# Optimization experiments

Hardware: AMD Instinct MI355X
Metric: run time of the kernel (lower is better)

The kernel has to match this reference:

```python
import jax, jax.numpy as jnp
import numpy as np

LN_EPS = 1e-5
BN_EPS = 1e-5
ALPHA = 0.1

def _layer_norm(x):
    # F.layer_norm over last dim, no affine
    mu = jnp.mean(x, axis=-1, keepdims=True)
    var = jnp.var(x, axis=-1, keepdims=True)
    return (x - mu) * jax.lax.rsqrt(var + LN_EPS)

def setup_inputs() -> dict:
    key = jax.random.key(0)
    ks = jax.random.split(key, 12)
    N, Nh, D, Dq = 8192, 8192, 64, 64
    s = 1.0 / np.sqrt(D)
    inp = {
        "X": jax.random.normal(ks[0], (N, D), jnp.float32),
        "H": jax.random.normal(ks[1], (Nh, D), jnp.float32),
        "M": jax.random.uniform(ks[2], (N, Nh), jnp.float32),
        # Linear params (torch nn.Linear: y = x @ W.T + b), uniform init scale
        "Qw": jax.random.uniform(ks[3], (Dq, D), jnp.float32, -s, s),
        "Qb": jax.random.uniform(ks[4], (Dq,), jnp.float32, -s, s),
        "Kw": jax.random.uniform(ks[5], (Dq, D), jnp.float32, -s, s),
        "Kb": jax.random.uniform(ks[6], (Dq,), jnp.float32, -s, s),
        "Vw": jax.random.uniform(ks[7], (64, D), jnp.float32, -s, s),
        "Vb": jax.random.uniform(ks[8], (64,), jnp.float32, -s, s),
        # BatchNorm1d(64) eval-mode params
        "bn_gamma": jnp.ones((64,), jnp.float32),
        "bn_beta": jnp.zeros((64,), jnp.float32),
        "bn_mean": 0.1 * jax.random.normal(ks[9], (64,), jnp.float32),
        "bn_var": jax.random.uniform(ks[10], (64,), jnp.float32, 0.5, 1.5),
    }
    return inp

def reference(X, H, M, Qw, Qb, Kw, Kb, Vw, Vb, bn_gamma, bn_beta, bn_mean, bn_var):
    # K/Q branches: Linear + LayerNorm
    K = _layer_norm(H @ Kw.T + Kb)            # [Nh, Dq]
    Q = _layer_norm(X @ Qw.T + Qb)            # [N, Dq]
    # V branch: Linear + BatchNorm1d (eval mode; dropout is identity in eval)
    V = (H @ Vw.T + Vb - bn_mean) * jax.lax.rsqrt(bn_var + BN_EPS) * bn_gamma + bn_beta  # [Nh, 64]
    # Masked attention, softmax over dim=0 (columns)
    A = (Q @ K.T) * 0.125                     # [N, Nh]
    A = jax.nn.softmax(M * A, axis=0)
    # globel=True branch
    return ALPHA * (A @ V) + M @ H            # [N, 64]
```

## Files before the change

kernel.cpp:

```cpp
#include <hip/hip_runtime.h>
#include <hip/hip_bf16.h>
#include <math.h>

#define NN 8192
#define QSCALE (0.125f * 1.44269504088896f)
#define OSZ (8192*64)
#define NSL 16

typedef __attribute__((ext_vector_type(8))) short short8;
typedef __attribute__((ext_vector_type(16))) float f32x16;
typedef __attribute__((ext_vector_type(4))) float f32x4;

union W4 { unsigned u[4]; short8 v; };

__device__ inline unsigned short f2bf(float x) {
  union { float f; unsigned u; } t; t.f = x;
  unsigned r = t.u + 0x7fffu + ((t.u >> 16) & 1u);
  return (unsigned short)(r >> 16);
}
__device__ inline unsigned cvtpk(float lo, float hi) {
  unsigned r;
  asm("v_cvt_pk_bf16_f32 %0, %1, %2" : "=v"(r) : "v"(lo), "v"(hi));
  return r;
}
__device__ inline float fexp2(float x) {
  float r;
  asm("v_exp_f32 %0, %1" : "=v"(r) : "v"(x));
  return r;
}
__device__ inline void gload16(const float* g, float* l) {
  __builtin_amdgcn_global_load_lds(
      (const __attribute__((address_space(1))) void*)g,
      (__attribute__((address_space(3))) void*)l, 16, 0, 0);
}

__global__ __launch_bounds__(256) void qkv_kernel(
    const float* __restrict__ X, const float* __restrict__ H,
    const float* __restrict__ Qw, const float* __restrict__ Qb,
    const float* __restrict__ Kw, const float* __restrict__ Kb,
    const float* __restrict__ Vw, const float* __restrict__ Vb,
    const float* __restrict__ bng, const float* __restrict__ bnb,
    const float* __restrict__ bnm, const float* __restrict__ bnv,
    unsigned short* __restrict__ QP, unsigned short* __restrict__ KP,
    unsigned short* __restrict__ VP, unsigned short* __restrict__ HP)
{
  int wid = (blockIdx.x * blockDim.x + threadIdx.x) >> 6;
  int d = threadIdx.x & 63;
  float4 w[16];

  for (int fq = 0; fq < 16; fq++) w[fq] = *(const float4*)(Qw + d*64 + fq*4);
  for (int rr = 0; rr < 4; rr++) {
    int r = wid*4 + rr;
    float a = Qb[d];
    for (int fq = 0; fq < 16; fq++) {
      float4 xv = *(const float4*)(X + r*64 + fq*4);
      a += w[fq].x*xv.x + w[fq].y*xv.y + w[fq].z*xv.z + w[fq].w*xv.w;
    }
    float s = a;
    for (int off = 32; off; off >>= 1) s += __shfl_xor(s, off);
    float mean = s * (1.f/64.f);
    float c = a - mean;
    float s2 = c*c;
    for (int off = 32; off; off >>= 1) s2 += __shfl_xor(s2, off);
    float q = c * rsqrtf(s2*(1.f/64.f) + 1e-5f);
    QP[(d>>3)*65536 + r*8 + (d&7)] = f2bf(q * QSCALE);
  }
  for (int fq = 0; fq < 16; fq++) w[fq] = *(const float4*)(Kw + d*64 + fq*4);
  for (int rr = 0; rr < 4; rr++) {
    int r = wid*4 + rr;
    float a = Kb[d];
    for (int fq = 0; fq < 16; fq++) {
      float4 hv = *(const float4*)(H + r*64 + fq*4);
      a += w[fq].x*hv.x + w[fq].y*hv.y + w[fq].z*hv.z + w[fq].w*hv.w;
    }
    float s = a;
    for (int off = 32; off; off >>= 1) s += __shfl_xor(s, off);
    float mean = s * (1.f/64.f);
    float c = a - mean;
    float s2 = c*c;
    for (int off = 32; off; off >>= 1) s2 += __shfl_xor(s2, off);
    float k = c * rsqrtf(s2*(1.f/64.f) + 1e-5f);
    KP[(d>>3)*65536 + r*8 + (d&7)] = f2bf(k);
  }
  for (int fq = 0; fq < 16; fq++) w[fq] = *(const float4*)(Vw + d*64 + fq*4);
  float bscale = rsqrtf(bnv[d] + 1e-5f) * bng[d];
  for (int rr = 0; rr < 4; rr++) {
    int r = wid*4 + rr;
    float a = Vb[d];
    for (int fq = 0; fq < 16; fq++) {
      float4 hv = *(const float4*)(H + r*64 + fq*4);
      a += w[fq].x*hv.x + w[fq].y*hv.y + w[fq].z*hv.z + w[fq].w*hv.w;
    }
    float v = (a - bnm[d]) * bscale + bnb[d];
    VP[(r>>3)*512 + d*8 + (r&7)] = f2bf(v);
    HP[(r>>3)*512 + d*8 + (r&7)] = f2bf(H[r*64 + d]);
  }
}

__global__ __launch_bounds__(256) void pass1_kernel(
    const float* __restrict__ M, const unsigned short* __restrict__ QP,
    const unsigned short* __restrict__ KP, float* __restrict__ pd)
{
  int tid = threadIdx.x;
  int wj = (blockIdx.x * blockDim.x + tid) >> 6;
  int lane = tid & 63;
  int l31 = lane & 31, h = lane >> 5;
  int jb = wj & 255, slice = wj >> 8;
  int j = jb*32 + l31;

  short8 kb[4];
  for (int m = 0; m < 4; m++)
    kb[m] = *(const short8*)(KP + (2*m + h)*65536 + j*8);

  float Mv[16];
  {
    int i0 = slice*8*32;
#pragma unroll
    for (int r = 0; r < 16; r++) {
      int ir = (r&3) + 8*(r>>2) + 4*h;
      Mv[r] = M[(size_t)(i0 + ir)*NN + j];
    }
  }

  float d0 = 0.f, d1 = 0.f, d2 = 0.f, d3 = 0.f;
  for (int t = 0; t < 8; t++) {
    int i0 = (slice*8 + t) * 32;
    float Mn[16];
    if (t < 7) {
      int i1 = i0 + 32;
#pragma unroll
      for (int r = 0; r < 16; r++) {
        int ir = (r&3) + 8*(r>>2) + 4*h;
        Mn[r] = M[(size_t)(i1 + ir)*NN + j];
      }
    }

    f32x16 acc;
    for (int r = 0; r < 16; r++) acc[r] = 0.f;
    __builtin_amdgcn_s_setprio(1);
    for (int m = 0; m < 4; m++) {
      short8 qa = *(const short8*)(QP + (2*m + h)*65536 + (size_t)(i0 + l31)*8);
      acc = __builtin_amdgcn_mfma_f32_32x32x16_bf16(qa, kb[m], acc, 0, 0, 0);
    }
    __builtin_amdgcn_s_setprio(0);

    d0 += fexp2(acc[0]*Mv[0]) + fexp2(acc[4]*Mv[4]) + fexp2(acc[8]*Mv[8])   + fexp2(acc[12]*Mv[12]);
    d1 += fexp2(acc[1]*Mv[1]) + fexp2(acc[5]*Mv[5]) + fexp2(acc[9]*Mv[9])   + fexp2(acc[13]*Mv[13]);
    d2 += fexp2(acc[2]*Mv[2]) + fexp2(acc[6]*Mv[6]) + fexp2(acc[10]*Mv[10]) + fexp2(acc[14]*Mv[14]);
    d3 += fexp2(acc[3]*Mv[3]) + fexp2(acc[7]*Mv[7]) + fexp2(acc[11]*Mv[11]) + fexp2(acc[15]*Mv[15]);

    if (t < 7) {
#pragma unroll
      for (int r = 0; r < 16; r++) Mv[r] = Mn[r];
    }
  }
  float drun = (d0 + d1) + (d2 + d3);
  drun += __shfl_xor(drun, 32);
  if (lane < 32) pd[(size_t)slice*NN + j] = drun;
}

__global__ __launch_bounds__(256) void cv_kernel(
    const float* __restrict__ pd, const unsigned short* __restrict__ VP,
    unsigned short* __restrict__ VP2)
{
  __shared__ float cls[256];
  int tid = threadIdx.x;
  int j = blockIdx.x * 256 + tid;
  float Dv = 0.f;
  for (int s = 0; s < 32; s++) Dv += pd[(size_t)s*NN + j];
  cls[tid] = 0.1f / Dv;
  __syncthreads();

  int base = blockIdx.x * 2048;
#pragma unroll
  for (int k = 0; k < 8; k++) {
    int idx = base + k*256 + tid;
    int lj8 = (k*256 + tid) >> 6;
    const unsigned short* src = VP + (size_t)idx*8;
    unsigned short sv[8];
    *(short8*)sv = *(const short8*)src;
    float f[8];
#pragma unroll
    for (int e = 0; e < 8; e++)
      f[e] = __uint_as_float(((unsigned)sv[e]) << 16) * cls[lj8*8 + e];
    W4 o;
    o.u[0] = cvtpk(f[0], f[1]); o.u[1] = cvtpk(f[2], f[3]);
    o.u[2] = cvtpk(f[4], f[5]); o.u[3] = cvtpk(f[6], f[7]);
    *(short8*)(VP2 + (size_t)idx*8) = o.v;
  }
}

__global__ __launch_bounds__(256) void pass2_kernel(
    const float* __restrict__ M, const unsigned short* __restrict__ QP,
    const unsigned short* __restrict__ KP, const unsigned short* __restrict__ VP2,
    const unsigned short* __restrict__ HP, float* __restrict__ opart)
{
  __shared__ __align__(16) float tile[2][128*32];

  int iblk = blockIdx.x >> 4, slice = blockIdx.x & 15;
  int i0 = iblk * 128;
  int tid = threadIdx.x;
  int lane = tid & 63, wv = tid >> 6;
  int l31 = lane & 31, h = lane >> 5;
  int irow = wv*32 + l31;
  int i_g = i0 + irow;
  int r7 = irow & 7;

  short8 qb[4];
#pragma unroll
  for (int m = 0; m < 4; m++)
    qb[m] = *(const short8*)(QP + (2*m + h)*65536 + (size_t)i_g*8);

  int rsub = lane >> 3;
  int gdst = lane & 7;
  int c0base = slice*512;

#pragma unroll
  for (int k = 0; k < 4; k++) {
    int rloc = wv*32 + k*8 + rsub;
    int gs = gdst ^ (rloc & 7);
    gload16(M + (size_t)(i0 + rloc)*NN + c0base + gs*4,
            &tile[0][(wv*32 + k*8)*32]);
  }

  f32x16 saccC;
  for (int r = 0; r < 16; r++) saccC[r] = 0.f;
  {
    short8 k0[4];
#pragma unroll
    for (int m = 0; m < 4; m++)
      k0[m] = *(const short8*)(KP + (2*m + h)*65536 + (size_t)(c0base + l31)*8);
    __builtin_amdgcn_s_setprio(1);
#pragma unroll
    for (int m = 0; m < 4; m++)
      saccC = __builtin_amdgcn_mfma_f32_32x32x16_bf16(k0[m], qb[m], saccC, 0, 0, 0);
    __builtin_amdgcn_s_setprio(0);
  }
  __syncthreads();

  f32x16 oaccA, oaccB;
  for (int r = 0; r < 16; r++) { oaccA[r] = 0.f; oaccB[r] = 0.f; }

  for (int tm = 0; tm < 16; tm++) {
    int jt = c0base + tm*32;

    if (tm < 15) {
      int c0 = c0base + (tm+1)*32;
      float* dst = tile[(tm+1) & 1];
#pragma unroll
      for (int k = 0; k < 4; k++) {
        int rloc = wv*32 + k*8 + rsub;
        int gs = gdst ^ (rloc & 7);
        gload16(M + (size_t)(i0 + rloc)*NN + c0 + gs*4,
                &dst[(wv*32 + k*8)*32]);
      }
    }
    const float* mb = tile[tm & 1];

    short8 knxt[4];
    if (tm < 15) {
#pragma unroll
      for (int m = 0; m < 4; m++)
        knxt[m] = *(const short8*)(KP + (2*m + h)*65536 + (size_t)(jt + 32 + l31)*8);
    }

    f32x4 mv[4];
#pragma unroll
    for (int q = 0; q < 4; q++) {
      int gr = 2*q + h;
      mv[q] = *(const f32x4*)&mb[irow*32 + ((gr ^ r7) << 2)];
    }

    float p[16];
#pragma unroll
    for (int q = 0; q < 4; q++) {
      p[4*q+0] = fexp2(saccC[4*q+0] * mv[q][0]);
      p[4*q+1] = fexp2(saccC[4*q+1] * mv[q][1]);
      p[4*q+2] = fexp2(saccC[4*q+2] * mv[q][2]);
      p[4*q+3] = fexp2(saccC[4*q+3] * mv[q][3]);
    }
    unsigned pu[8], mw[8];
#pragma unroll
    for (int k = 0; k < 8; k++) pu[k] = cvtpk(p[2*k], p[2*k+1]);
#pragma unroll
    for (int q = 0; q < 4; q++) {
      mw[2*q]   = cvtpk(mv[q][0], mv[q][1]);
      mw[2*q+1] = cvtpk(mv[q][2], mv[q][3]);
    }

    asm volatile("v_permlane32_swap_b32 %0, %1" : "+v"(pu[0]), "+v"(pu[2]));
    asm volatile("v_permlane32_swap_b32 %0, %1" : "+v"(pu[1]), "+v"(pu[3]));
    asm volatile("v_permlane32_swap_b32 %0, %1" : "+v"(pu[4]), "+v"(pu[6]));
    asm volatile("v_permlane32_swap_b32 %0, %1" : "+v"(pu[5]), "+v"(pu[7]));
    asm volatile("v_permlane32_swap_b32 %0, %1" : "+v"(mw[0]), "+v"(mw[2]));
    asm volatile("v_permlane32_swap_b32 %0, %1" : "+v"(mw[1]), "+v"(mw[3]));
    asm volatile("v_permlane32_swap_b32 %0, %1" : "+v"(mw[4]), "+v"(mw[6]));
    asm volatile("v_permlane32_swap_b32 %0, %1" : "+v"(mw[5]), "+v"(mw[7]));

    W4 PA0, PA1, MA0, MA1;
    PA0.u[0] = pu[0]; PA0.u[1] = pu[1]; PA0.u[2] = pu[2]; PA0.u[3] = pu[3];
    PA1.u[0] = pu[4]; PA1.u[1] = pu[5]; PA1.u[2] = pu[6]; PA1.u[3] = pu[7];
    MA0.u[0] = mw[0]; MA0.u[1] = mw[1]; MA0.u[2] = mw[2]; MA0.u[3] = mw[3];
    MA1.u[0] = mw[4]; MA1.u[1] = mw[5]; MA1.u[2] = mw[6]; MA1.u[3] = mw[7];

    int j8 = jt >> 3;
    const unsigned short* vb_ = VP2 + (size_t)j8*512 + l31*8;
    const unsigned short* hb_ = HP  + (size_t)j8*512 + l31*8;
    {
      short8 vA1 = *(const short8*)(vb_ + h*512);
      short8 vA2 = *(const short8*)(vb_ + (2 + h)*512);
      short8 hA1 = *(const short8*)(hb_ + h*512);
      short8 hA2 = *(const short8*)(hb_ + (2 + h)*512);
      short8 vB1 = *(const short8*)(vb_ + 256 + h*512);
      short8 vB2 = *(const short8*)(vb_ + 256 + (2 + h)*512);
      short8 hB1 = *(const short8*)(hb_ + 256 + h*512);
      short8 hB2 = *(const short8*)(hb_ + 256 + (2 + h)*512);
      __builtin_amdgcn_s_setprio(1);
      oaccA = __builtin_amdgcn_mfma_f32_32x32x16_bf16(PA0.v, vA1, oaccA, 0, 0, 0);
      oaccB = __builtin_amdgcn_mfma_f32_32x32x16_bf16(PA0.v, vB1, oaccB, 0, 0, 0);
      oaccA = __builtin_amdgcn_mfma_f32_32x32x16_bf16(PA1.v, vA2, oaccA, 0, 0, 0);
      oaccB = __builtin_amdgcn_mfma_f32_32x32x16_bf16(PA1.v, vB2, oaccB, 0, 0, 0);
      oaccA = __builtin_amdgcn_mfma_f32_32x32x16_bf16(MA0.v, hA1, oaccA, 0, 0, 0);
      oaccB = __builtin_amdgcn_mfma_f32_32x32x16_bf16(MA0.v, hB1, oaccB, 0, 0, 0);
      oaccA = __builtin_amdgcn_mfma_f32_32x32x16_bf16(MA1.v, hA2, oaccA, 0, 0, 0);
      oaccB = __builtin_amdgcn_mfma_f32_32x32x16_bf16(MA1.v, hB2, oaccB, 0, 0, 0);
      __builtin_amdgcn_s_setprio(0);
    }

    if (tm < 15) {
      for (int r = 0; r < 16; r++) saccC[r] = 0.f;
      __builtin_amdgcn_s_setprio(1);
#pragma unroll
      for (int m = 0; m < 4; m++)
        saccC = __builtin_amdgcn_mfma_f32_32x32x16_bf16(knxt[m], qb[m], saccC, 0, 0, 0);
      __builtin_amdgcn_s_setprio(0);
    }

    __syncthreads();
  }

  float* obase = opart + (size_t)slice*OSZ;
#pragma unroll
  for (int r = 0; r < 16; r++) {
    int orow = i0 + wv*32 + (r&3) + 8*(r>>2) + 4*h;
    obase[(size_t)orow*64 + l31]      = oaccA[r];
    obase[(size_t)orow*64 + 32 + l31] = oaccB[r];
  }
}

__global__ __launch_bounds__(256) void reduce_kernel(
    const float* __restrict__ opart, float* __restrict__ out)
{
  int e4 = blockIdx.x * blockDim.x + threadIdx.x;
  const float4* p = (const float4*)opart;
  float4 a = p[e4];
#pragma unroll
  for (int s = 1; s < NSL; s++) {
    float4 b = p[(size_t)s*(OSZ/4) + e4];
    a.x += b.x; a.y += b.y; a.z += b.z; a.w += b.w;
  }
  ((float4*)out)[e4] = a;
}

extern "C" void kernel_launch(void* const* d_in, const int* in_sizes, int n_in,
                              void* d_out, int out_size, void* d_ws, size_t ws_size,
                              hipStream_t stream) {
  const float* X   = (const float*)d_in[0];
  const float* H   = (const float*)d_in[1];
  const float* M   = (const float*)d_in[2];
  const float* Qw  = (const float*)d_in[3];
  const float* Qb  = (const float*)d_in[4];
  const float* Kw  = (const float*)d_in[5];
  const float* Kb  = (const float*)d_in[6];
  const float* Vw  = (const float*)d_in[7];
  const float* Vb  = (const float*)d_in[8];
  const float* bng = (const float*)d_in[9];
  const float* bnb = (const float*)d_in[10];
  const float* bnm = (const float*)d_in[11];
  const float* bnv = (const float*)d_in[12];
  float* out = (float*)d_out;

  char* ws = (char*)d_ws;
  const size_t MB = 1024*1024;
  unsigned short* QP  = (unsigned short*)(ws);
  unsigned short* KP  = (unsigned short*)(ws + 1*MB);
  unsigned short* VP  = (unsigned short*)(ws + 2*MB);
  unsigned short* HP  = (unsigned short*)(ws + 3*MB);
  unsigned short* VP2 = (unsigned short*)(ws + 4*MB);
  float* pd           = (float*)(ws + 5*MB);
  float* opart        = (float*)(ws + 7*MB);

  qkv_kernel<<<512, 256, 0, stream>>>(X, H, Qw, Qb, Kw, Kb, Vw, Vb,
                                      bng, bnb, bnm, bnv, QP, KP, VP, HP);
  pass1_kernel<<<2048, 256, 0, stream>>>(M, QP, KP, pd);
  cv_kernel<<<32, 256, 0, stream>>>(pd, VP, VP2);
  pass2_kernel<<<1024, 256, 0, stream>>>(M, QP, KP, VP2, HP, opart);
  reduce_kernel<<<512, 256, 0, stream>>>(opart, out);
}
```

Measured before the change: 165.5 us.

## Make M tile staging per-wave and drop block-wide barriers in pass2

Splits the shared M tile into separate per-wave double buffers, since each wave only reads the 32 rows it loaded. The per-iteration __syncthreads is replaced by a wave-local vmcnt wait followed by a sched barrier. The next tile's M values are read from LDS one iteration early, and the V/H operand loads are issued before the exp work so their latency is hidden. The risk is relying on vmcnt alone to order the async global-to-LDS loads against the LDS reads within a wave, and waiting on vmcnt(0) also stalls on the prefetched K and V/H loads.

```diff
diff --git a/kernel.cpp b/kernel.cpp
--- a/kernel.cpp
+++ b/kernel.cpp
@@ -195,7 +195,7 @@
     const unsigned short* __restrict__ KP, const unsigned short* __restrict__ VP2,
     const unsigned short* __restrict__ HP, float* __restrict__ opart)
 {
-  __shared__ __align__(16) float tile[2][128*32];
+  __shared__ __align__(16) float tile[4][2][32*32];
 
   int iblk = blockIdx.x >> 4, slice = blockIdx.x & 15;
   int i0 = iblk * 128;
@@ -204,7 +204,7 @@
   int l31 = lane & 31, h = lane >> 5;
   int irow = wv*32 + l31;
   int i_g = i0 + irow;
-  int r7 = irow & 7;
+  int r7 = l31 & 7;
 
   short8 qb[4];
 #pragma unroll
@@ -214,15 +214,14 @@
   int rsub = lane >> 3;
   int gdst = lane & 7;
   int c0base = slice*512;
+  const float* mwave = M + (size_t)(i0 + wv*32)*NN;
 
 #pragma unroll
   for (int k = 0; k < 4; k++) {
-    int rloc = wv*32 + k*8 + rsub;
-    int gs = gdst ^ (rloc & 7);
-    gload16(M + (size_t)(i0 + rloc)*NN + c0base + gs*4,
-            &tile[0][(wv*32 + k*8)*32]);
-  }
-
+    int lr = k*8 + rsub;
+    int gs = gdst ^ (lr & 7);
+    gload16(mwave + (size_t)lr*NN + c0base + gs*4, &tile[wv][0][(k*8)*32]);
+  }
   f32x16 saccC;
   for (int r = 0; r < 16; r++) saccC[r] = 0.f;
   {
@@ -236,7 +235,14 @@
       saccC = __builtin_amdgcn_mfma_f32_32x32x16_bf16(k0[m], qb[m], saccC, 0, 0, 0);
     __builtin_amdgcn_s_setprio(0);
   }
-  __syncthreads();
+  asm volatile("s_waitcnt vmcnt(0)" ::: "memory");
+  __builtin_amdgcn_sched_barrier(0);
+  f32x4 mvC[4];
+#pragma unroll
+  for (int q = 0; q < 4; q++) {
+    int gr = 2*q + h;
+    mvC[q] = *(const f32x4*)&tile[wv][0][l31*32 + ((gr ^ r7) << 2)];
+  }
 
   f32x16 oaccA, oaccB;
   for (int r = 0; r < 16; r++) { oaccA[r] = 0.f; oaccB[r] = 0.f; }
@@ -246,16 +252,14 @@
 
     if (tm < 15) {
       int c0 = c0base + (tm+1)*32;
-      float* dst = tile[(tm+1) & 1];
+      float* dst = &tile[wv][(tm+1) & 1][0];
 #pragma unroll
       for (int k = 0; k < 4; k++) {
-        int rloc = wv*32 + k*8 + rsub;
-        int gs = gdst ^ (rloc & 7);
-        gload16(M + (size_t)(i0 + rloc)*NN + c0 + gs*4,
-                &dst[(wv*32 + k*8)*32]);
+        int lr = k*8 + rsub;
+        int gs = gdst ^ (lr & 7);
+        gload16(mwave + (size_t)lr*NN + c0 + gs*4, &dst[(k*8)*32]);
       }
     }
-    const float* mb = tile[tm & 1];
 
     short8 knxt[4];
     if (tm < 15) {
@@ -264,28 +268,33 @@
         knxt[m] = *(const short8*)(KP + (2*m + h)*65536 + (size_t)(jt + 32 + l31)*8);
     }
 
-    f32x4 mv[4];
+    int j8 = jt >> 3;
+    const unsigned short* vb_ = VP2 + (size_t)j8*512 + l31*8;
+    const unsigned short* hb_ = HP  + (size_t)j8*512 + l31*8;
+    short8 vA1 = *(const short8*)(vb_ + h*512);
+    short8 vA2 = *(const short8*)(vb_ + (2 + h)*512);
+    short8 hA1 = *(const short8*)(hb_ + h*512);
+    short8 hA2 = *(const short8*)(hb_ + (2 + h)*512);
+    short8 vB1 = *(const short8*)(vb_ + 256 + h*512);
+    short8 vB2 = *(const short8*)(vb_ + 256 + (2 + h)*512);
+    short8 hB1 = *(const short8*)(hb_ + 256 + h*512);
+    short8 hB2 = *(const short8*)(hb_ + 256 + (2 + h)*512);
+
+    float p[16];
 #pragma unroll
     for (int q = 0; q < 4; q++) {
-      int gr = 2*q + h;
-      mv[q] = *(const f32x4*)&mb[irow*32 + ((gr ^ r7) << 2)];
-    }
-
-    float p[16];
+      p[4*q+0] = fexp2(saccC[4*q+0] * mvC[q][0]);
+      p[4*q+1] = fexp2(saccC[4*q+1] * mvC[q][1]);
+      p[4*q+2] = fexp2(saccC[4*q+2] * mvC[q][2]);
+      p[4*q+3] = fexp2(saccC[4*q+3] * mvC[q][3]);
+    }
+    unsigned pu[8], mw[8];
+#pragma unroll
+    for (int k = 0; k < 8; k++) pu[k] = cvtpk(p[2*k], p[2*k+1]);
 #pragma unroll
     for (int q = 0; q < 4; q++) {
-      p[4*q+0] = fexp2(saccC[4*q+0] * mv[q][0]);
-      p[4*q+1] = fexp2(saccC[4*q+1] * mv[q][1]);
-      p[4*q+2] = fexp2(saccC[4*q+2] * mv[q][2]);
-      p[4*q+3] = fexp2(saccC[4*q+3] * mv[q][3]);
-    }
-    unsigned pu[8], mw[8];
-#pragma unroll
-    for (int k = 0; k < 8; k++) pu[k] = cvtpk(p[2*k], p[2*k+1]);
-#pragma unroll
-    for (int q = 0; q < 4; q++) {
-      mw[2*q]   = cvtpk(mv[q][0], mv[q][1]);
-      mw[2*q+1] = cvtpk(mv[q][2], mv[q][3]);
+      mw[2*q]   = cvtpk(mvC[q][0], mvC[q][1]);
+      mw[2*q+1] = cvtpk(mvC[q][2], mvC[q][3]);
     }
 
     asm volatile("v_permlane32_swap_b32 %0, %1" : "+v"(pu[0]), "+v"(pu[2]));
@@ -303,31 +312,26 @@
     MA0.u[0] = mw[0]; MA0.u[1] = mw[1]; MA0.u[2] = mw[2]; MA0.u[3] = mw[3];
     MA1.u[0] = mw[4]; MA1.u[1] = mw[5]; MA1.u[2] = mw[6]; MA1.u[3] = mw[7];
 
-    int j8 = jt >> 3;
-    const unsigned short* vb_ = VP2 + (size_t)j8*512 + l31*8;
-    const unsigned short* hb_ = HP  + (size_t)j8*512 + l31*8;
-    {
-      short8 vA1 = *(const short8*)(vb_ + h*512);
-      short8 vA2 = *(const short8*)(vb_ + (2 + h)*512);
-      short8 hA1 = *(const short8*)(hb_ + h*512);
-      short8 hA2 = *(const short8*)(hb_ + (2 + h)*512);
-      short8 vB1 = *(const short8*)(vb_ + 256 + h*512);
-      short8 vB2 = *(const short8*)(vb_ + 256 + (2 + h)*512);
-      short8 hB1 = *(const short8*)(hb_ + 256 + h*512);
-      short8 hB2 = *(const short8*)(hb_ + 256 + (2 + h)*512);
-      __builtin_amdgcn_s_setprio(1);
-      oaccA = __builtin_amdgcn_mfma_f32_32x32x16_bf16(PA0.v, vA1, oaccA, 0, 0, 0);
-      oaccB = __builtin_amdgcn_mfma_f32_32x32x16_bf16(PA0.v, vB1, oaccB, 0, 0, 0);
-      oaccA = __builtin_amdgcn_mfma_f32_32x32x16_bf16(PA1.v, vA2, oaccA, 0, 0, 0);
-      oaccB = __builtin_amdgcn_mfma_f32_32x32x16_bf16(PA1.v, vB2, oaccB, 0, 0, 0);
-      oaccA = __builtin_amdgcn_mfma_f32_32x32x16_bf16(MA0.v, hA1, oaccA, 0, 0, 0);
-      oaccB = __builtin_amdgcn_mfma_f32_32x32x16_bf16(MA0.v, hB1, oaccB, 0, 0, 0);
-      oaccA = __builtin_amdgcn_mfma_f32_32x32x16_bf16(MA1.v, hA2, oaccA, 0, 0, 0);
-      oaccB = __builtin_amdgcn_mfma_f32_32x32x16_bf16(MA1.v, hB2, oaccB, 0, 0, 0);
-      __builtin_amdgcn_s_setprio(0);
-    }
+    __builtin_amdgcn_s_setprio(1);
+    oaccA = __builtin_amdgcn_mfma_f32_32x32x16_bf16(PA0.v, vA1, oaccA, 0, 0, 0);
+    oaccB = __builtin_amdgcn_mfma_f32_32x32x16_bf16(PA0.v, vB1, oaccB, 0, 0, 0);
+    oaccA = __builtin_amdgcn_mfma_f32_32x32x16_bf16(PA1.v, vA2, oaccA, 0, 0, 0);
+    oaccB = __builtin_amdgcn_mfma_f32_32x32x16_bf16(PA1.v, vB2, oaccB, 0, 0, 0);
+    oaccA = __builtin_amdgcn_mfma_f32_32x32x16_bf16(MA0.v, hA1, oaccA, 0, 0, 0);
+    oaccB = __builtin_amdgcn_mfma_f32_32x32x16_bf16(MA0.v, hB1, oaccB, 0, 0, 0);
+    oaccA = __builtin_amdgcn_mfma_f32_32x32x16_bf16(MA1.v, hA2, oaccA, 0, 0, 0);
+    oaccB = __builtin_amdgcn_mfma_f32_32x32x16_bf16(MA1.v, hB2, oaccB, 0, 0, 0);
+    __builtin_amdgcn_s_setprio(0);
 
     if (tm < 15) {
+      asm volatile("s_waitcnt vmcnt(0)" ::: "memory");
+      __builtin_amdgcn_sched_barrier(0);
+      const float* nb = &tile[wv][(tm+1) & 1][0];
+#pragma unroll
+      for (int q = 0; q < 4; q++) {
+        int gr = 2*q + h;
+        mvC[q] = *(const f32x4*)&nb[l31*32 + ((gr ^ r7) << 2)];
+      }
       for (int r = 0; r < 16; r++) saccC[r] = 0.f;
       __builtin_amdgcn_s_setprio(1);
 #pragma unroll
@@ -335,8 +339,6 @@
         saccC = __builtin_amdgcn_mfma_f32_32x32x16_bf16(knxt[m], qb[m], saccC, 0, 0, 0);
       __builtin_amdgcn_s_setprio(0);
     }
-
-    __syncthreads();
   }
 
   float* obase = opart + (size_t)slice*OSZ;
```

Measured after the change: 168.7 us. No clear change (+2.0%).
